# Kernel optimization log

Measured on AMD Instinct MI355X. Metric: run time of the kernel, lower is better.

Reference implementation:

```python
import jax, jax.numpy as jnp
import numpy as np

N, T, D_ENC, D_DEC, U = 32, 2048, 1024, 1024, 1024


def setup_inputs() -> dict:
    key = jax.random.key(0)
    k1, k2, k3, k4, k5, k6 = jax.random.split(key, 6)
    queries = jax.random.normal(k1, (N, 1, D_DEC), dtype=jnp.float32)
    encoder_output = jax.random.normal(k2, (N, T, D_ENC), dtype=jnp.float32)
    # lengths in [1, T] so every row has at least one valid position
    lengths = jax.random.randint(k3, (N,), 1, T + 1, dtype=jnp.int32)
    v = jax.random.normal(k4, (U,), dtype=jnp.float32)
    # torch Linear weights are [out, in]; y = x @ W.T
    Wq = jax.random.normal(k5, (U, D_DEC), dtype=jnp.float32) * (1.0 / np.sqrt(D_DEC))
    Wk = jax.random.normal(k6, (U, D_ENC), dtype=jnp.float32) * (1.0 / np.sqrt(D_ENC))
    return {"queries": queries, "encoder_output": encoder_output,
            "lengths": lengths, "v": v, "Wq": Wq, "Wk": Wk}


def reference(queries, encoder_output, lengths, v, Wq, Wk):
    # set_memory: project keys, build padding mask
    proj_key = jnp.einsum('nte,ue->ntu', encoder_output, Wk)      # [N,T,U]
    mask = jnp.arange(T)[None, :] >= lengths[:, None]             # [N,T] True = masked

    # forward (normalize=False path)
    proj_query = jnp.einsum('nqd,ud->nqu', queries, Wq)           # [N,1,U]
    weights = jnp.tanh(proj_query + proj_key) @ v                 # [N,T]
    weights = jnp.where(mask, -jnp.inf, weights)
    alignments = jax.nn.softmax(weights, axis=-1)                 # [N,T]
    contexts = jnp.einsum('nt,nte->ne', alignments, encoder_output)  # [N,D_enc]
    return contexts, alignments
```

## Files before the change

### kernel.cpp

```cpp
#include <hip/hip_runtime.h>
#include <hip/hip_bf16.h>

#define NB 32
#define TD 2048
#define DIM 1024

typedef _Float16 v8h __attribute__((ext_vector_type(8)));
typedef _Float16 v4h __attribute__((ext_vector_type(4)));
typedef float    v4f __attribute__((ext_vector_type(4)));

__device__ __forceinline__ float ftanh(float x) {
    x = fminf(15.f, fmaxf(-15.f, x));
    float e = __expf(2.f * x);
    return (e - 1.f) / (e + 1.f);
}

__device__ __forceinline__ void gld_lds16(const void* g, void* l) {
    __builtin_amdgcn_global_load_lds(
        (const __attribute__((address_space(1))) unsigned int*)g,
        (__attribute__((address_space(3))) unsigned int*)l, 16, 0, 0);
}

__global__ __launch_bounds__(256) void pq_kernel(const float* __restrict__ q,
                                                 const float* __restrict__ Wq,
                                                 float* __restrict__ pq) {
    int wid  = blockIdx.x * 4 + (threadIdx.x >> 6);
    int lane = threadIdx.x & 63;
    int n = wid >> 10;
    int u = wid & 1023;
    const float4* qr = (const float4*)(q  + (size_t)n * DIM);
    const float4* wr = (const float4*)(Wq + (size_t)u * DIM);
    float s = 0.f;
#pragma unroll
    for (int j = 0; j < 4; ++j) {
        int i = lane + 64 * j;
        float4 a = qr[i], b = wr[i];
        s += a.x * b.x + a.y * b.y + a.z * b.z + a.w * b.w;
    }
#pragma unroll
    for (int off = 32; off >= 1; off >>= 1) s += __shfl_xor(s, off);
    if (lane == 0) pq[(size_t)n * DIM + u] = s;
}

__global__ __launch_bounds__(256) void cvt_kernel(const float* __restrict__ enc,
                                                  const float* __restrict__ Wk,
                                                  const int* __restrict__ lengths,
                                                  _Float16* __restrict__ ench,
                                                  _Float16* __restrict__ wkh) {
    int local = threadIdx.x * 8;
    int rsub  = local >> 10;
    int col   = local & 1023;
    const float* src;
    _Float16* dst;
    size_t row;
    if (blockIdx.x < 32768) {
        row = (size_t)blockIdx.x * 2 + rsub;
        int n = (int)(row >> 11), t = (int)(row & 2047);
        if (t >= lengths[n]) return;
        src = enc; dst = ench;
    } else {
        row = (size_t)(blockIdx.x - 32768) * 2 + rsub;
        src = Wk; dst = wkh;
    }
    const float4* s = (const float4*)(src + row * DIM + col);
    float4 a = s[0], b = s[1];
    v8h h;
    h[0] = (_Float16)a.x; h[1] = (_Float16)a.y; h[2] = (_Float16)a.z; h[3] = (_Float16)a.w;
    h[4] = (_Float16)b.x; h[5] = (_Float16)b.y; h[6] = (_Float16)b.z; h[7] = (_Float16)b.w;
    *(v8h*)(dst + row * DIM + col) = h;
}

__global__ __launch_bounds__(256) void gemm_tanh_h(
        const _Float16* __restrict__ ench, const _Float16* __restrict__ wkh,
        const float* __restrict__ pq, const float* __restrict__ v,
        const int* __restrict__ lengths, float* __restrict__ weights) {
    const int bm = blockIdx.x;
    const int bn = blockIdx.y;
    const int rowBase = bm * 128;
    const int n = rowBase >> 11;
    const int tstart = rowBase & 2047;
    if (lengths[n] <= tstart) return;

    __shared__ _Float16 As[128 * 32];
    __shared__ _Float16 Bs[128 * 32];

    const int tid  = threadIdx.x;
    const int lane = tid & 63;
    const int wv   = tid >> 6;
    const int wm   = wv >> 1, wn = wv & 1;
    const int q4   = lane >> 4;
    const int l16  = lane & 15;

    v4f acc[4][4];
    const v4f vz = {0.f, 0.f, 0.f, 0.f};
#pragma unroll
    for (int i = 0; i < 4; ++i)
#pragma unroll
        for (int j = 0; j < 4; ++j) acc[i][j] = vz;

    const int srow = (lane >> 2);
    const int skc  = (lane & 3) * 8;
    const _Float16* Ag = ench + (size_t)rowBase * DIM;
    const _Float16* Bg = wkh + (size_t)bn * 128 * DIM;

    for (int k0 = 0; k0 < DIM; k0 += 32) {
        __syncthreads();
#pragma unroll
        for (int j = 0; j < 2; ++j) {
            int row = wv * 32 + j * 16 + srow;
            gld_lds16(Ag + (size_t)row * DIM + k0 + skc, &As[wv * 1024 + j * 512]);
            gld_lds16(Bg + (size_t)row * DIM + k0 + skc, &Bs[wv * 1024 + j * 512]);
        }
        __syncthreads();

        v8h afr[4], bfr[4];
#pragma unroll
        for (int mt = 0; mt < 4; ++mt)
            afr[mt] = *(const v8h*)(&As[(wm * 64 + mt * 16 + l16) * 32 + q4 * 8]);
#pragma unroll
        for (int nt = 0; nt < 4; ++nt)
            bfr[nt] = *(const v8h*)(&Bs[(wn * 64 + nt * 16 + l16) * 32 + q4 * 8]);
#pragma unroll
        for (int mt = 0; mt < 4; ++mt)
#pragma unroll
            for (int nt = 0; nt < 4; ++nt)
                acc[mt][nt] = __builtin_amdgcn_mfma_f32_16x16x32_f16(
                    afr[mt], bfr[nt], acc[mt][nt], 0, 0, 0);
    }

    float pqv[4], vv[4];
#pragma unroll
    for (int nt = 0; nt < 4; ++nt) {
        int ug = bn * 128 + wn * 64 + nt * 16 + l16;
        pqv[nt] = pq[(size_t)n * DIM + ug];
        vv[nt]  = v[ug];
    }
#pragma unroll
    for (int mt = 0; mt < 4; ++mt) {
#pragma unroll
        for (int r = 0; r < 4; ++r) {
            float s = 0.f;
#pragma unroll
            for (int nt = 0; nt < 4; ++nt)
                s += ftanh(acc[mt][nt][r] + pqv[nt]) * vv[nt];
            s += __shfl_xor(s, 1);
            s += __shfl_xor(s, 2);
            s += __shfl_xor(s, 4);
            s += __shfl_xor(s, 8);
            if (l16 == 0) {
                int R = rowBase + wm * 64 + mt * 16 + q4 * 4 + r;
                atomicAdd(&weights[R], s);
            }
        }
    }
}

__global__ __launch_bounds__(256) void gemm_tanh_kernel(
        const float* __restrict__ enc, const float* __restrict__ Wk,
        const float* __restrict__ pq,  const float* __restrict__ v,
        const int* __restrict__ lengths, float* __restrict__ weights) {
    const int bm = blockIdx.x;
    const int bn = blockIdx.y;
    const int rowBase = bm * 128;
    const int n = rowBase >> 11;
    const int tstart = rowBase & 2047;
    if (lengths[n] <= tstart) return;

    __shared__ _Float16 As[128 * 40];
    __shared__ _Float16 Bs[128 * 40];

    const int tid  = threadIdx.x;
    const int lane = tid & 63;
    const int wv   = tid >> 6;
    const int wm   = wv >> 1, wn = wv & 1;
    const int q4   = lane >> 4;
    const int l16  = lane & 15;

    v4f acc[4][4];
    const v4f vz = {0.f, 0.f, 0.f, 0.f};
#pragma unroll
    for (int i = 0; i < 4; ++i)
#pragma unroll
        for (int j = 0; j < 4; ++j) acc[i][j] = vz;

    const int srow = tid >> 3;
    const int skc  = (tid & 7) * 4;

    for (int k0 = 0; k0 < DIM; k0 += 32) {
        __syncthreads();
#pragma unroll
        for (int j = 0; j < 4; ++j) {
            int row = j * 32 + srow;
            float4 av = *(const float4*)(enc + (size_t)(rowBase + row) * DIM + k0 + skc);
            v4h ah;
            ah.x = (_Float16)av.x; ah.y = (_Float16)av.y;
            ah.z = (_Float16)av.z; ah.w = (_Float16)av.w;
            *(v4h*)(&As[row * 40 + skc]) = ah;
            float4 bv = *(const float4*)(Wk + (size_t)(bn * 128 + row) * DIM + k0 + skc);
            v4h bh;
            bh.x = (_Float16)bv.x; bh.y = (_Float16)bv.y;
            bh.z = (_Float16)bv.z; bh.w = (_Float16)bv.w;
            *(v4h*)(&Bs[row * 40 + skc]) = bh;
        }
        __syncthreads();

        v8h afr[4], bfr[4];
#pragma unroll
        for (int mt = 0; mt < 4; ++mt)
            afr[mt] = *(const v8h*)(&As[(wm * 64 + mt * 16 + l16) * 40 + q4 * 8]);
#pragma unroll
        for (int nt = 0; nt < 4; ++nt)
            bfr[nt] = *(const v8h*)(&Bs[(wn * 64 + nt * 16 + l16) * 40 + q4 * 8]);
#pragma unroll
        for (int mt = 0; mt < 4; ++mt)
#pragma unroll
            for (int nt = 0; nt < 4; ++nt)
                acc[mt][nt] = __builtin_amdgcn_mfma_f32_16x16x32_f16(
                    afr[mt], bfr[nt], acc[mt][nt], 0, 0, 0);
    }

    float pqv[4], vv[4];
#pragma unroll
    for (int nt = 0; nt < 4; ++nt) {
        int ug = bn * 128 + wn * 64 + nt * 16 + l16;
        pqv[nt] = pq[(size_t)n * DIM + ug];
        vv[nt]  = v[ug];
    }
#pragma unroll
    for (int mt = 0; mt < 4; ++mt) {
#pragma unroll
        for (int r = 0; r < 4; ++r) {
            float s = 0.f;
#pragma unroll
            for (int nt = 0; nt < 4; ++nt)
                s += ftanh(acc[mt][nt][r] + pqv[nt]) * vv[nt];
            s += __shfl_xor(s, 1);
            s += __shfl_xor(s, 2);
            s += __shfl_xor(s, 4);
            s += __shfl_xor(s, 8);
            if (l16 == 0) {
                int R = rowBase + wm * 64 + mt * 16 + q4 * 4 + r;
                atomicAdd(&weights[R], s);
            }
        }
    }
}

__global__ __launch_bounds__(256) void softmax_kernel(float* __restrict__ w,
                                                      const int* __restrict__ lengths) {
    int n = blockIdx.x;
    int len = lengths[n];
    float* row = w + (size_t)n * TD;
    int tid = threadIdx.x;
    float wv[8], ev[8];
    float mx = -INFINITY;
#pragma unroll
    for (int i = 0; i < 8; ++i) {
        int t = tid + i * 256;
        float x = row[t];
        x = (t < len) ? x : -INFINITY;
        wv[i] = x;
        mx = fmaxf(mx, x);
    }
#pragma unroll
    for (int off = 32; off >= 1; off >>= 1) mx = fmaxf(mx, __shfl_xor(mx, off));
    __shared__ float redm[4], reds[4];
    int lane = tid & 63, wvid = tid >> 6;
    if (lane == 0) redm[wvid] = mx;
    __syncthreads();
    mx = fmaxf(fmaxf(redm[0], redm[1]), fmaxf(redm[2], redm[3]));
    float sm = 0.f;
#pragma unroll
    for (int i = 0; i < 8; ++i) { ev[i] = __expf(wv[i] - mx); sm += ev[i]; }
#pragma unroll
    for (int off = 32; off >= 1; off >>= 1) sm += __shfl_xor(sm, off);
    if (lane == 0) reds[wvid] = sm;
    __syncthreads();
    sm = reds[0] + reds[1] + reds[2] + reds[3];
    float inv = 1.f / sm;
#pragma unroll
    for (int i = 0; i < 8; ++i) row[tid + i * 256] = ev[i] * inv;
}

__global__ __launch_bounds__(256) void ctx_kernel_h(const float* __restrict__ align,
                                                    const _Float16* __restrict__ ench,
                                                    const int* __restrict__ lengths,
                                                    float* __restrict__ ctx) {
    int n  = blockIdx.y;
    int t0 = blockIdx.x * 32;
    int len = lengths[n];
    if (len <= t0) return;
    int e = threadIdx.x * 4;
    float4 acc = make_float4(0.f, 0.f, 0.f, 0.f);
    const float* arow = align + (size_t)n * TD;
    const _Float16* erow = ench + (size_t)n * TD * DIM;
    int tend = min(t0 + 32, len);
    for (int t = t0; t < tend; ++t) {
        float a = arow[t];
        v4h ev = *(const v4h*)(erow + (size_t)t * DIM + e);
        acc.x += a * (float)ev[0]; acc.y += a * (float)ev[1];
        acc.z += a * (float)ev[2]; acc.w += a * (float)ev[3];
    }
    float* c = ctx + (size_t)n * DIM + e;
    atomicAdd(c + 0, acc.x);
    atomicAdd(c + 1, acc.y);
    atomicAdd(c + 2, acc.z);
    atomicAdd(c + 3, acc.w);
}

__global__ __launch_bounds__(256) void ctx_kernel(const float* __restrict__ align,
                                                  const float* __restrict__ enc,
                                                  const int* __restrict__ lengths,
                                                  float* __restrict__ ctx) {
    int n  = blockIdx.y;
    int t0 = blockIdx.x * 128;
    if (lengths[n] <= t0) return;
    int e = threadIdx.x * 4;
    float4 acc = make_float4(0.f, 0.f, 0.f, 0.f);
    const float* arow = align + (size_t)n * TD;
    const float* erow = enc + (size_t)n * TD * DIM;
    for (int tt = 0; tt < 128; ++tt) {
        int t = t0 + tt;
        float a = arow[t];
        if (a != 0.f) {
            float4 evv = *(const float4*)(erow + (size_t)t * DIM + e);
            acc.x += a * evv.x; acc.y += a * evv.y;
            acc.z += a * evv.z; acc.w += a * evv.w;
        }
    }
    float* c = ctx + (size_t)n * DIM + e;
    atomicAdd(c + 0, acc.x);
    atomicAdd(c + 1, acc.y);
    atomicAdd(c + 2, acc.z);
    atomicAdd(c + 3, acc.w);
}

extern "C" void kernel_launch(void* const* d_in, const int* in_sizes, int n_in,
                              void* d_out, int out_size, void* d_ws, size_t ws_size,
                              hipStream_t stream) {
    const float* queries = (const float*)d_in[0];
    const float* enc     = (const float*)d_in[1];
    const int*   lengths = (const int*)d_in[2];
    const float* v       = (const float*)d_in[3];
    const float* Wq      = (const float*)d_in[4];
    const float* Wk      = (const float*)d_in[5];

    float* out = (float*)d_out;
    float* ctx = out;
    float* alg = out + NB * DIM;
    float* pq  = ctx;
    (void)in_sizes; (void)n_in; (void)out_size;

    const size_t ench_elems = (size_t)NB * TD * DIM;
    const size_t need = (ench_elems + (size_t)DIM * DIM) * sizeof(_Float16);

    hipMemsetAsync(alg, 0, (size_t)NB * TD * sizeof(float), stream);
    pq_kernel<<<NB * DIM / 4, 256, 0, stream>>>(queries, Wq, pq);

    if (ws_size >= need) {
        _Float16* ench = (_Float16*)d_ws;
        _Float16* wkh  = ench + ench_elems;
        cvt_kernel<<<32768 + 512, 256, 0, stream>>>(enc, Wk, lengths, ench, wkh);
        dim3 g2(512, 8);
        gemm_tanh_h<<<g2, 256, 0, stream>>>(ench, wkh, pq, v, lengths, alg);
        softmax_kernel<<<NB, 256, 0, stream>>>(alg, lengths);
        hipMemsetAsync(ctx, 0, (size_t)NB * DIM * sizeof(float), stream);
        ctx_kernel_h<<<dim3(64, NB), 256, 0, stream>>>(alg, ench, lengths, ctx);
    } else {
        dim3 g2(512, 8);
        gemm_tanh_kernel<<<g2, 256, 0, stream>>>(enc, Wk, pq, v, lengths, alg);
        softmax_kernel<<<NB, 256, 0, stream>>>(alg, lengths);
        hipMemsetAsync(ctx, 0, (size_t)NB * DIM * sizeof(float), stream);
        ctx_kernel<<<dim3(16, NB), 256, 0, stream>>>(alg, enc, lengths, ctx);
    }
}
```

Measured before the change: 572.9 us.

## Loop all N tiles per block in tanh GEMM with double-buffered swizzled LDS

The fp16 tanh-GEMM kernel now has each block walk all eight 128-wide U tiles itself instead of using a 2-D grid. It double-buffers 64-wide K slices in XOR-swizzled LDS and caches pq and v in shared memory. Partial tanh·v sums stay in registers and are reduced across waves through LDS, so each weight is written directly. That removes the atomics and the memset of the weights buffer. The context kernel now covers 256 timesteps per block with 8-wide fp16 loads and an in-block reduction, which cuts atomic traffic. The cost is a smaller grid (512 blocks) with heavier LDS use, which may leave compute units underused because many blocks exit early on padded rows.

```diff
diff --git a/kernel.cpp b/kernel.cpp
--- a/kernel.cpp
+++ b/kernel.cpp
@@ -70,19 +70,22 @@
     *(v8h*)(dst + row * DIM + col) = h;
 }
 
-__global__ __launch_bounds__(256) void gemm_tanh_h(
+#define NIT 128
+__global__ __launch_bounds__(256) void gemm_tanh_h2(
         const _Float16* __restrict__ ench, const _Float16* __restrict__ wkh,
         const float* __restrict__ pq, const float* __restrict__ v,
         const int* __restrict__ lengths, float* __restrict__ weights) {
     const int bm = blockIdx.x;
-    const int bn = blockIdx.y;
     const int rowBase = bm * 128;
     const int n = rowBase >> 11;
     const int tstart = rowBase & 2047;
     if (lengths[n] <= tstart) return;
 
-    __shared__ _Float16 As[128 * 32];
-    __shared__ _Float16 Bs[128 * 32];
+    __shared__ _Float16 As[2][128 * 64];
+    __shared__ _Float16 Bs[2][128 * 64];
+    __shared__ float pq_s[DIM];
+    __shared__ float v_s[DIM];
+    __shared__ float wred[128];
 
     const int tid  = threadIdx.x;
     const int lane = tid & 63;
@@ -91,67 +94,132 @@
     const int q4   = lane >> 4;
     const int l16  = lane & 15;
 
+    const int sr  = lane >> 3;
+    const int scs = (lane & 7) ^ sr;
+
+    const _Float16* Abase = ench + (size_t)(rowBase + wv * 32 + sr) * DIM + scs * 8;
+    const _Float16* Bbase = wkh + (size_t)(wv * 32 + sr) * DIM + scs * 8;
+
     v4f acc[4][4];
+    float wacc[4][4];
     const v4f vz = {0.f, 0.f, 0.f, 0.f};
 #pragma unroll
     for (int i = 0; i < 4; ++i)
 #pragma unroll
-        for (int j = 0; j < 4; ++j) acc[i][j] = vz;
-
-    const int srow = (lane >> 2);
-    const int skc  = (lane & 3) * 8;
-    const _Float16* Ag = ench + (size_t)rowBase * DIM;
-    const _Float16* Bg = wkh + (size_t)bn * 128 * DIM;
-
-    for (int k0 = 0; k0 < DIM; k0 += 32) {
-        __syncthreads();
-#pragma unroll
-        for (int j = 0; j < 2; ++j) {
-            int row = wv * 32 + j * 16 + srow;
-            gld_lds16(Ag + (size_t)row * DIM + k0 + skc, &As[wv * 1024 + j * 512]);
-            gld_lds16(Bg + (size_t)row * DIM + k0 + skc, &Bs[wv * 1024 + j * 512]);
-        }
-        __syncthreads();
-
-        v8h afr[4], bfr[4];
-#pragma unroll
-        for (int mt = 0; mt < 4; ++mt)
-            afr[mt] = *(const v8h*)(&As[(wm * 64 + mt * 16 + l16) * 32 + q4 * 8]);
-#pragma unroll
-        for (int nt = 0; nt < 4; ++nt)
-            bfr[nt] = *(const v8h*)(&Bs[(wn * 64 + nt * 16 + l16) * 32 + q4 * 8]);
-#pragma unroll
-        for (int mt = 0; mt < 4; ++mt)
-#pragma unroll
-            for (int nt = 0; nt < 4; ++nt)
-                acc[mt][nt] = __builtin_amdgcn_mfma_f32_16x16x32_f16(
-                    afr[mt], bfr[nt], acc[mt][nt], 0, 0, 0);
-    }
-
-    float pqv[4], vv[4];
-#pragma unroll
-    for (int nt = 0; nt < 4; ++nt) {
-        int ug = bn * 128 + wn * 64 + nt * 16 + l16;
-        pqv[nt] = pq[(size_t)n * DIM + ug];
-        vv[nt]  = v[ug];
-    }
-#pragma unroll
-    for (int mt = 0; mt < 4; ++mt) {
+        for (int j = 0; j < 4; ++j) { acc[i][j] = vz; wacc[i][j] = 0.f; }
+
+    auto STAGE = [&](int it, int buf) {
+        const int bn = it >> 4;
+        const int k0 = (it & 15) << 6;
+        const _Float16* Ap = Abase + k0;
+        const _Float16* Bp = Bbase + (size_t)bn * (128 * DIM) + k0;
+        _Float16* Al = &As[buf][(wv * 32) * 64];
+        _Float16* Bl = &Bs[buf][(wv * 32) * 64];
+#pragma unroll
+        for (int j = 0; j < 4; ++j) {
+            gld_lds16(Ap + j * 8 * DIM, Al + j * 8 * 64);
+            gld_lds16(Bp + j * 8 * DIM, Bl + j * 8 * 64);
+        }
+    };
+
+#pragma unroll
+    for (int i = tid; i < DIM; i += 256) {
+        pq_s[i] = pq[(size_t)n * DIM + i];
+        v_s[i]  = v[i];
+    }
+    STAGE(0, 0);
+    __syncthreads();
+
+    for (int it = 0; it < NIT; ++it) {
+        const int buf = it & 1;
+        if (it + 1 < NIT) {
+            STAGE(it + 1, buf ^ 1);
+            asm volatile("s_waitcnt vmcnt(8)" ::: "memory");
+        } else {
+            asm volatile("s_waitcnt vmcnt(0)" ::: "memory");
+        }
+        __builtin_amdgcn_sched_barrier(0);
+        __builtin_amdgcn_s_barrier();
+        __builtin_amdgcn_sched_barrier(0);
+
+#pragma unroll
+        for (int kk = 0; kk < 2; ++kk) {
+            v8h a[4], b[4];
+#pragma unroll
+            for (int mt = 0; mt < 4; ++mt) {
+                int r = wm * 64 + mt * 16 + l16;
+                a[mt] = *(const v8h*)(&As[buf][r * 64 + (((kk * 4 + q4) ^ (r & 7)) * 8)]);
+            }
+#pragma unroll
+            for (int nt = 0; nt < 4; ++nt) {
+                int r = wn * 64 + nt * 16 + l16;
+                b[nt] = *(const v8h*)(&Bs[buf][r * 64 + (((kk * 4 + q4) ^ (r & 7)) * 8)]);
+            }
+#pragma unroll
+            for (int mt = 0; mt < 4; ++mt)
+#pragma unroll
+                for (int nt = 0; nt < 4; ++nt)
+                    acc[mt][nt] = __builtin_amdgcn_mfma_f32_16x16x32_f16(
+                        a[mt], b[nt], acc[mt][nt], 0, 0, 0);
+        }
+
+        if ((it & 15) == 15) {
+            const int bn = it >> 4;
+            float pqv[4], vv[4];
+#pragma unroll
+            for (int nt = 0; nt < 4; ++nt) {
+                int ug = bn * 128 + wn * 64 + nt * 16 + l16;
+                pqv[nt] = pq_s[ug];
+                vv[nt]  = v_s[ug];
+            }
+#pragma unroll
+            for (int mt = 0; mt < 4; ++mt)
+#pragma unroll
+                for (int r = 0; r < 4; ++r) {
+                    float s = 0.f;
+#pragma unroll
+                    for (int nt = 0; nt < 4; ++nt)
+                        s += ftanh(acc[mt][nt][r] + pqv[nt]) * vv[nt];
+                    wacc[mt][r] += s;
+                }
+#pragma unroll
+            for (int mt = 0; mt < 4; ++mt)
+#pragma unroll
+                for (int nt = 0; nt < 4; ++nt) acc[mt][nt] = vz;
+        }
+
+        __builtin_amdgcn_sched_barrier(0);
+        __builtin_amdgcn_s_barrier();
+        __builtin_amdgcn_sched_barrier(0);
+    }
+
+#pragma unroll
+    for (int mt = 0; mt < 4; ++mt)
 #pragma unroll
         for (int r = 0; r < 4; ++r) {
-            float s = 0.f;
-#pragma unroll
-            for (int nt = 0; nt < 4; ++nt)
-                s += ftanh(acc[mt][nt][r] + pqv[nt]) * vv[nt];
+            float s = wacc[mt][r];
             s += __shfl_xor(s, 1);
             s += __shfl_xor(s, 2);
             s += __shfl_xor(s, 4);
             s += __shfl_xor(s, 8);
-            if (l16 == 0) {
+            wacc[mt][r] = s;
+        }
+    if (wn == 1 && l16 == 0) {
+#pragma unroll
+        for (int mt = 0; mt < 4; ++mt)
+#pragma unroll
+            for (int r = 0; r < 4; ++r)
+                wred[wm * 64 + mt * 16 + q4 * 4 + r] = wacc[mt][r];
+    }
+    __syncthreads();
+    if (wn == 0 && l16 == 0) {
+#pragma unroll
+        for (int mt = 0; mt < 4; ++mt)
+#pragma unroll
+            for (int r = 0; r < 4; ++r) {
                 int R = rowBase + wm * 64 + mt * 16 + q4 * 4 + r;
-                atomicAdd(&weights[R], s);
+                weights[R] = wacc[mt][r] + wred[wm * 64 + mt * 16 + q4 * 4 + r];
             }
-        }
     }
 }
 
@@ -282,30 +350,39 @@
     for (int i = 0; i < 8; ++i) row[tid + i * 256] = ev[i] * inv;
 }
 
-__global__ __launch_bounds__(256) void ctx_kernel_h(const float* __restrict__ align,
-                                                    const _Float16* __restrict__ ench,
-                                                    const int* __restrict__ lengths,
-                                                    float* __restrict__ ctx) {
+__global__ __launch_bounds__(256) void ctx_kernel_h2(const float* __restrict__ align,
+                                                     const _Float16* __restrict__ ench,
+                                                     const int* __restrict__ lengths,
+                                                     float* __restrict__ ctx) {
     int n  = blockIdx.y;
-    int t0 = blockIdx.x * 32;
+    int t0 = blockIdx.x * 256;
     int len = lengths[n];
     if (len <= t0) return;
-    int e = threadIdx.x * 4;
-    float4 acc = make_float4(0.f, 0.f, 0.f, 0.f);
+    int half = threadIdx.x >> 7;
+    int col  = (threadIdx.x & 127) * 8;
+    float acc[8];
+#pragma unroll
+    for (int i = 0; i < 8; ++i) acc[i] = 0.f;
+    int tend = min(t0 + 256, len);
     const float* arow = align + (size_t)n * TD;
-    const _Float16* erow = ench + (size_t)n * TD * DIM;
-    int tend = min(t0 + 32, len);
-    for (int t = t0; t < tend; ++t) {
+    const _Float16* ebase = ench + (size_t)n * TD * DIM + col;
+    for (int t = t0 + half; t < tend; t += 2) {
         float a = arow[t];
-        v4h ev = *(const v4h*)(erow + (size_t)t * DIM + e);
-        acc.x += a * (float)ev[0]; acc.y += a * (float)ev[1];
-        acc.z += a * (float)ev[2]; acc.w += a * (float)ev[3];
-    }
-    float* c = ctx + (size_t)n * DIM + e;
-    atomicAdd(c + 0, acc.x);
-    atomicAdd(c + 1, acc.y);
-    atomicAdd(c + 2, acc.z);
-    atomicAdd(c + 3, acc.w);
+        v8h e = *(const v8h*)(ebase + (size_t)t * DIM);
+#pragma unroll
+        for (int i = 0; i < 8; ++i) acc[i] += a * (float)e[i];
+    }
+    __shared__ float cred[DIM];
+    if (half == 1) {
+#pragma unroll
+        for (int i = 0; i < 8; ++i) cred[col + i] = acc[i];
+    }
+    __syncthreads();
+    if (half == 0) {
+        float* c = ctx + (size_t)n * DIM + col;
+#pragma unroll
+        for (int i = 0; i < 8; ++i) atomicAdd(c + i, acc[i] + cred[col + i]);
+    }
 }
 
 __global__ __launch_bounds__(256) void ctx_kernel(const float* __restrict__ align,
@@ -354,19 +431,18 @@
     const size_t ench_elems = (size_t)NB * TD * DIM;
     const size_t need = (ench_elems + (size_t)DIM * DIM) * sizeof(_Float16);
 
-    hipMemsetAsync(alg, 0, (size_t)NB * TD * sizeof(float), stream);
     pq_kernel<<<NB * DIM / 4, 256, 0, stream>>>(queries, Wq, pq);
 
     if (ws_size >= need) {
         _Float16* ench = (_Float16*)d_ws;
         _Float16* wkh  = ench + ench_elems;
         cvt_kernel<<<32768 + 512, 256, 0, stream>>>(enc, Wk, lengths, ench, wkh);
-        dim3 g2(512, 8);
-        gemm_tanh_h<<<g2, 256, 0, stream>>>(ench, wkh, pq, v, lengths, alg);
+        gemm_tanh_h2<<<512, 256, 0, stream>>>(ench, wkh, pq, v, lengths, alg);
         softmax_kernel<<<NB, 256, 0, stream>>>(alg, lengths);
         hipMemsetAsync(ctx, 0, (size_t)NB * DIM * sizeof(float), stream);
-        ctx_kernel_h<<<dim3(64, NB), 256, 0, stream>>>(alg, ench, lengths, ctx);
+        ctx_kernel_h2<<<dim3(8, NB), 256, 0, stream>>>(alg, ench, lengths, ctx);
     } else {
+        hipMemsetAsync(alg, 0, (size_t)NB * TD * sizeof(float), stream);
         dim3 g2(512, 8);
         gemm_tanh_kernel<<<g2, 256, 0, stream>>>(enc, Wk, pq, v, lengths, alg);
         softmax_kernel<<<NB, 256, 0, stream>>>(alg, lengths);
```

Measured after the change: 612.4 us. +6.9%, slower.

## Widen GEMM K-tile with XOR-swizzled LDS, remap blocks per XCD, restructure context kernel

Applied to the files above, without the earlier changes.

The tanh GEMM now stages 64-wide K slices per iteration, which halves the number of barrier pairs. It uses an XOR swizzle on LDS columns to avoid bank conflicts on fragment reads. Blocks go into a 1D grid remapped so that consecutive M tiles on the same XCD share B tiles and L2. The context kernel handles 128 timesteps per block with 8-wide fp16 loads, reduces two halves through shared memory, and issues a quarter as many atomics. The trade-offs are more LDS per block and a different grid shape, which may change occupancy.

```diff
diff --git a/kernel.cpp b/kernel.cpp
--- a/kernel.cpp
+++ b/kernel.cpp
@@ -70,19 +70,22 @@
     *(v8h*)(dst + row * DIM + col) = h;
 }
 
-__global__ __launch_bounds__(256) void gemm_tanh_h(
+__global__ __launch_bounds__(256) void gemm_tanh_h3(
         const _Float16* __restrict__ ench, const _Float16* __restrict__ wkh,
         const float* __restrict__ pq, const float* __restrict__ v,
         const int* __restrict__ lengths, float* __restrict__ weights) {
-    const int bm = blockIdx.x;
-    const int bn = blockIdx.y;
+    const int bid = blockIdx.x;
+    const int xcd = bid & 7;
+    const int idx = bid >> 3;
+    const int bm  = ((idx >> 3) << 3) | xcd;
+    const int bn  = idx & 7;
     const int rowBase = bm * 128;
     const int n = rowBase >> 11;
     const int tstart = rowBase & 2047;
     if (lengths[n] <= tstart) return;
 
-    __shared__ _Float16 As[128 * 32];
-    __shared__ _Float16 Bs[128 * 32];
+    __shared__ _Float16 As[128 * 64];
+    __shared__ _Float16 Bs[128 * 64];
 
     const int tid  = threadIdx.x;
     const int lane = tid & 63;
@@ -91,6 +94,14 @@
     const int q4   = lane >> 4;
     const int l16  = lane & 15;
 
+    const int sr  = lane >> 3;
+    const int scs = (lane & 7) ^ sr;
+
+    const _Float16* Ag = ench + (size_t)(rowBase + wv * 32 + sr) * DIM + scs * 8;
+    const _Float16* Bg = wkh + (size_t)(bn * 128 + wv * 32 + sr) * DIM + scs * 8;
+    _Float16* Al = &As[(wv * 32) * 64];
+    _Float16* Bl = &Bs[(wv * 32) * 64];
+
     v4f acc[4][4];
     const v4f vz = {0.f, 0.f, 0.f, 0.f};
 #pragma unroll
@@ -98,34 +109,35 @@
 #pragma unroll
         for (int j = 0; j < 4; ++j) acc[i][j] = vz;
 
-    const int srow = (lane >> 2);
-    const int skc  = (lane & 3) * 8;
-    const _Float16* Ag = ench + (size_t)rowBase * DIM;
-    const _Float16* Bg = wkh + (size_t)bn * 128 * DIM;
-
-    for (int k0 = 0; k0 < DIM; k0 += 32) {
+    for (int k0 = 0; k0 < DIM; k0 += 64) {
         __syncthreads();
 #pragma unroll
-        for (int j = 0; j < 2; ++j) {
-            int row = wv * 32 + j * 16 + srow;
-            gld_lds16(Ag + (size_t)row * DIM + k0 + skc, &As[wv * 1024 + j * 512]);
-            gld_lds16(Bg + (size_t)row * DIM + k0 + skc, &Bs[wv * 1024 + j * 512]);
+        for (int j = 0; j < 4; ++j) {
+            gld_lds16(Ag + k0 + j * 8 * DIM, Al + j * 8 * 64);
+            gld_lds16(Bg + k0 + j * 8 * DIM, Bl + j * 8 * 64);
         }
         __syncthreads();
 
-        v8h afr[4], bfr[4];
-#pragma unroll
-        for (int mt = 0; mt < 4; ++mt)
-            afr[mt] = *(const v8h*)(&As[(wm * 64 + mt * 16 + l16) * 32 + q4 * 8]);
-#pragma unroll
-        for (int nt = 0; nt < 4; ++nt)
-            bfr[nt] = *(const v8h*)(&Bs[(wn * 64 + nt * 16 + l16) * 32 + q4 * 8]);
-#pragma unroll
-        for (int mt = 0; mt < 4; ++mt)
-#pragma unroll
-            for (int nt = 0; nt < 4; ++nt)
-                acc[mt][nt] = __builtin_amdgcn_mfma_f32_16x16x32_f16(
-                    afr[mt], bfr[nt], acc[mt][nt], 0, 0, 0);
+#pragma unroll
+        for (int kk = 0; kk < 2; ++kk) {
+            v8h a[4], b[4];
+#pragma unroll
+            for (int mt = 0; mt < 4; ++mt) {
+                int r = wm * 64 + mt * 16 + l16;
+                a[mt] = *(const v8h*)(&As[r * 64 + (((kk * 4 + q4) ^ (r & 7)) * 8)]);
+            }
+#pragma unroll
+            for (int nt = 0; nt < 4; ++nt) {
+                int r = wn * 64 + nt * 16 + l16;
+                b[nt] = *(const v8h*)(&Bs[r * 64 + (((kk * 4 + q4) ^ (r & 7)) * 8)]);
+            }
+#pragma unroll
+            for (int mt = 0; mt < 4; ++mt)
+#pragma unroll
+                for (int nt = 0; nt < 4; ++nt)
+                    acc[mt][nt] = __builtin_amdgcn_mfma_f32_16x16x32_f16(
+                        a[mt], b[nt], acc[mt][nt], 0, 0, 0);
+        }
     }
 
     float pqv[4], vv[4];
@@ -282,30 +294,39 @@
     for (int i = 0; i < 8; ++i) row[tid + i * 256] = ev[i] * inv;
 }
 
-__global__ __launch_bounds__(256) void ctx_kernel_h(const float* __restrict__ align,
-                                                    const _Float16* __restrict__ ench,
-                                                    const int* __restrict__ lengths,
-                                                    float* __restrict__ ctx) {
+__global__ __launch_bounds__(256) void ctx_kernel_h3(const float* __restrict__ align,
+                                                     const _Float16* __restrict__ ench,
+                                                     const int* __restrict__ lengths,
+                                                     float* __restrict__ ctx) {
     int n  = blockIdx.y;
-    int t0 = blockIdx.x * 32;
+    int t0 = blockIdx.x * 128;
     int len = lengths[n];
     if (len <= t0) return;
-    int e = threadIdx.x * 4;
-    float4 acc = make_float4(0.f, 0.f, 0.f, 0.f);
+    int half = threadIdx.x >> 7;
+    int col  = (threadIdx.x & 127) * 8;
+    float acc[8];
+#pragma unroll
+    for (int i = 0; i < 8; ++i) acc[i] = 0.f;
+    int tend = min(t0 + 128, len);
     const float* arow = align + (size_t)n * TD;
-    const _Float16* erow = ench + (size_t)n * TD * DIM;
-    int tend = min(t0 + 32, len);
-    for (int t = t0; t < tend; ++t) {
+    const _Float16* ebase = ench + (size_t)n * TD * DIM + col;
+    for (int t = t0 + half; t < tend; t += 2) {
         float a = arow[t];
-        v4h ev = *(const v4h*)(erow + (size_t)t * DIM + e);
-        acc.x += a * (float)ev[0]; acc.y += a * (float)ev[1];
-        acc.z += a * (float)ev[2]; acc.w += a * (float)ev[3];
-    }
-    float* c = ctx + (size_t)n * DIM + e;
-    atomicAdd(c + 0, acc.x);
-    atomicAdd(c + 1, acc.y);
-    atomicAdd(c + 2, acc.z);
-    atomicAdd(c + 3, acc.w);
+        v8h e = *(const v8h*)(ebase + (size_t)t * DIM);
+#pragma unroll
+        for (int i = 0; i < 8; ++i) acc[i] += a * (float)e[i];
+    }
+    __shared__ float cred[DIM];
+    if (half == 1) {
+#pragma unroll
+        for (int i = 0; i < 8; ++i) cred[col + i] = acc[i];
+    }
+    __syncthreads();
+    if (half == 0) {
+        float* c = ctx + (size_t)n * DIM + col;
+#pragma unroll
+        for (int i = 0; i < 8; ++i) atomicAdd(c + i, acc[i] + cred[col + i]);
+    }
 }
 
 __global__ __launch_bounds__(256) void ctx_kernel(const float* __restrict__ align,
@@ -361,11 +382,10 @@
         _Float16* ench = (_Float16*)d_ws;
         _Float16* wkh  = ench + ench_elems;
         cvt_kernel<<<32768 + 512, 256, 0, stream>>>(enc, Wk, lengths, ench, wkh);
-        dim3 g2(512, 8);
-        gemm_tanh_h<<<g2, 256, 0, stream>>>(ench, wkh, pq, v, lengths, alg);
+        gemm_tanh_h3<<<4096, 256, 0, stream>>>(ench, wkh, pq, v, lengths, alg);
         softmax_kernel<<<NB, 256, 0, stream>>>(alg, lengths);
         hipMemsetAsync(ctx, 0, (size_t)NB * DIM * sizeof(float), stream);
-        ctx_kernel_h<<<dim3(64, NB), 256, 0, stream>>>(alg, ench, lengths, ctx);
+        ctx_kernel_h3<<<dim3(16, NB), 256, 0, stream>>>(alg, ench, lengths, ctx);
     } else {
         dim3 g2(512, 8);
         gemm_tanh_kernel<<<g2, 256, 0, stream>>>(enc, Wk, pq, v, lengths, alg);
```

Result: faster. 517.7 us (-9.6%).
